# Kernel optimization log

Measured on AMD Instinct MI355X. Metric: run time of the kernel, lower is better.

Reference implementation:

```python
import jax, jax.numpy as jnp
import numpy as np

B, S, D, H, NS = 4, 4096, 1024, 16, 128
DA, DF = 512, 4096
DK, DV = DA // H, D // H  # 32, 64
TEMP = 1.0
EPS = 1e-6


def setup_inputs() -> dict:
    key = jax.random.key(0)
    ks = jax.random.split(key, 8)
    r = lambda k, shp: jax.random.normal(k, shp, jnp.float32) * 0.02
    return dict(
        x=jax.random.normal(ks[0], (B, S, D), jnp.float32),
        mask=jnp.ones((B, S), jnp.float32),
        residual_scale=jnp.ones((1,), jnp.float32),
        w_q=r(ks[1], (D, DA)), b_q=jnp.zeros((DA,), jnp.float32),
        w_kv=r(ks[2], (D, DA + D)), b_kv=jnp.zeros((DA + D,), jnp.float32),
        w_s=r(ks[3], (D, H * NS)), b_s=jnp.zeros((H * NS,), jnp.float32),
        w_cat=r(ks[4], (D, D)), b_cat=jnp.zeros((D,), jnp.float32),
        norm1_w=jnp.ones((D,), jnp.float32), norm2_w=jnp.ones((D,), jnp.float32),
        w1=r(ks[5], (D, DF)), b1=jnp.zeros((DF,), jnp.float32),
        w2=r(ks[6], (DF, D)), b2=jnp.zeros((D,), jnp.float32),
    )


def _rms(x, w):
    return x * jax.lax.rsqrt(jnp.mean(x * x, axis=-1, keepdims=True) + EPS) * w


def _forward(x, mask, residual_scale, w_q, b_q, w_kv, b_kv, w_s, b_s,
             w_cat, b_cat, norm1_w, norm2_w, w1, b1, w2, b2):
    neg = jnp.finfo(jnp.float32).min
    xn = _rms(x, norm1_w)
    q = (xn @ w_q + b_q).reshape(B, S, H, DK).transpose(0, 2, 1, 3)        # [B,H,S,DK]
    kv = (xn @ w_kv + b_kv).reshape(B, S, H, DK + DV).transpose(0, 2, 1, 3)  # [B,H,S,DK+DV]
    k_raw, v_raw = kv[..., :DK], kv[..., DK:]

    # DSZRC sampler: per-head soft routing of S tokens -> NS sampled KV rows
    logits = (x @ w_s + b_s).reshape(B, S, H, NS).transpose(0, 2, 3, 1)    # [B,H,NS,S]
    logits = jnp.where(mask[:, None, None, :] > 0, logits, neg)
    probs = jax.nn.softmax(logits / TEMP, axis=-1)
    kv_s = jnp.einsum('bhms,bhsd->bhmd', probs, kv)                        # [B,H,NS,DK+DV]
    k_s, v_s = kv_s[..., :DK], kv_s[..., DK:]

    # branch 1: dense SDPA over sampled KV
    scale = 1.0 / np.sqrt(DK).astype(np.float32)
    att = jax.nn.softmax(jnp.einsum('bhqd,bhkd->bhqk', q, k_s) * scale, axis=-1)
    out1 = jnp.einsum('bhqk,bhkd->bhqd', att, v_s)                         # [B,H,S,DV]

    # branch 2: fp16 sliding-window flash attn, left window = NS (keys i-NS..i)
    f16 = lambda t: t.astype(jnp.float16).astype(jnp.float32)
    qh, kh, vh = f16(q), f16(k_raw), f16(v_raw)
    bs = NS
    nb = S // bs
    qb = qh.reshape(B, H, nb, bs, DK)
    kb = kh.reshape(B, H, nb, bs, DK)
    vb = vh.reshape(B, H, nb, bs, DV)
    shift = lambda t: jnp.concatenate([jnp.zeros_like(t[:, :, :1]), t[:, :, :-1]], axis=2)
    kctx = jnp.concatenate([shift(kb), kb], axis=3)                        # [B,H,nb,2bs,DK]
    vctx = jnp.concatenate([shift(vb), vb], axis=3)
    sc = jnp.einsum('bhnad,bhnkd->bhnak', qb, kctx) * scale                # [B,H,nb,bs,2bs]
    a = jnp.arange(bs)[:, None]
    bcol = jnp.arange(2 * bs)[None, :]
    band = (bcol >= a) & (bcol <= a + NS)                                  # 0 <= q-k <= NS
    tpos = jnp.arange(nb)[:, None, None]
    valid = band[None] & ((tpos > 0) | (bcol >= bs)[None])                 # no keys before pos 0
    p = jax.nn.softmax(jnp.where(valid[None, None], sc, neg), axis=-1)
    out2 = f16(jnp.einsum('bhnak,bhnkd->bhnad', p, vctx)).reshape(B, H, S, DV)

    x_att = (out1 + out2).transpose(0, 2, 1, 3).reshape(B, S, D)
    x = x + (x_att @ w_cat + b_cat) * residual_scale
    h = _rms(x, norm2_w)
    x = x + (jax.nn.gelu(h @ w1 + b1, approximate=False) @ w2 + b2) * residual_scale
    return x


def reference(x, mask, residual_scale, w_q, b_q, w_kv, b_kv, w_s, b_s,
              w_cat, b_cat, norm1_w, norm2_w, w1, b1, w2, b2):
    return _forward(x, mask, residual_scale, w_q, b_q, w_kv, b_kv, w_s, b_s,
                    w_cat, b_cat, norm1_w, norm2_w, w1, b1, w2, b2)
```

## Files before the change

kernel.cpp:

```cpp
#include <hip/hip_runtime.h>
#include <cstdint>
#include <cmath>

#define DEV __device__ __forceinline__

using f16 = _Float16;
typedef f16  f16x4 __attribute__((ext_vector_type(4)));
typedef f16  f16x8 __attribute__((ext_vector_type(8)));
typedef float f32x4 __attribute__((ext_vector_type(4)));

constexpr int Bq = 4, Sq = 4096, Hq = 16;
constexpr int Tq = Bq * Sq;

DEV void gload_lds16(const void* g, void* l) {
  __builtin_amdgcn_global_load_lds(
      (const __attribute__((address_space(1))) void*)g,
      (__attribute__((address_space(3))) void*)l, 16, 0, 0);
}

DEV void stage_swz(const char* gbase, long gstride, char* lds, int nbytes,
                   int rowlog, int swzmask) {
  int tid = threadIdx.x;
  for (int b0 = 0; b0 < nbytes; b0 += 4096) {
    int P = b0 + tid * 16;
    int L = P ^ (((P >> rowlog) & swzmask) << 4);
    long row  = L >> rowlog;
    int  colb = L & ((1 << rowlog) - 1);
    gload_lds16(gbase + row * gstride + colb, lds + b0 + (tid & ~63) * 16);
  }
}

DEV void stage_swz512(const char* gbase, long gstride, char* lds, int nbytes,
                      int rowlog, int swzmask) {
  int tid = threadIdx.x;
  for (int b0 = 0; b0 < nbytes; b0 += 8192) {
    int P = b0 + tid * 16;
    int L = P ^ (((P >> rowlog) & swzmask) << 4);
    long row  = L >> rowlog;
    int  colb = L & ((1 << rowlog) - 1);
    gload_lds16(gbase + row * gstride + colb, lds + b0 + (tid & ~63) * 16);
  }
}

DEV float wave16_max(float v) {
#pragma unroll
  for (int d = 1; d < 16; d <<= 1) v = fmaxf(v, __shfl_xor(v, d, 64));
  return v;
}
DEV float wave16_sum(float v) {
#pragma unroll
  for (int d = 1; d < 16; d <<= 1) v += __shfl_xor(v, d, 64);
  return v;
}

__global__ __launch_bounds__(256) void wcast_k(const float* __restrict__ W,
                                               f16* __restrict__ Wt, int K, int N) {
  int n0 = blockIdx.x * 32, k0 = blockIdx.y * 32;
  __shared__ float tile[32][33];
  int tid = threadIdx.x, r = tid >> 5, c = tid & 31;
#pragma unroll
  for (int i = 0; i < 4; ++i)
    tile[r + i * 8][c] = W[(size_t)(k0 + r + i * 8) * N + n0 + c];
  __syncthreads();
#pragma unroll
  for (int i = 0; i < 4; ++i) {
    int rr = r + i * 8;
    Wt[(size_t)(n0 + rr) * K + k0 + c] = (f16)tile[c][rr];
  }
}

__global__ void bias_concat_k(const float* __restrict__ bq, const float* __restrict__ bkv,
                              float* __restrict__ out) {
  int i = blockIdx.x * 256 + threadIdx.x;
  out[i] = (i < 512) ? bq[i] : bkv[i - 512];
}

__global__ __launch_bounds__(256) void rmsnorm_k(const float* __restrict__ x,
                                                 const float* __restrict__ w,
                                                 f16* __restrict__ xn) {
  int row = blockIdx.x, tid = threadIdx.x;
  float4 v = ((const float4*)(x + (size_t)row * 1024))[tid];
  float ss = v.x * v.x + v.y * v.y + v.z * v.z + v.w * v.w;
#pragma unroll
  for (int d = 1; d < 64; d <<= 1) ss += __shfl_xor(ss, d, 64);
  __shared__ float red[4];
  if ((tid & 63) == 0) red[tid >> 6] = ss;
  __syncthreads();
  float tot = red[0] + red[1] + red[2] + red[3];
  float r = rsqrtf(tot * (1.0f / 1024.0f) + 1e-6f);
  float4 wv = ((const float4*)w)[tid];
  f16x4 o;
  o[0] = (f16)(v.x * r * wv.x); o[1] = (f16)(v.y * r * wv.y);
  o[2] = (f16)(v.z * r * wv.z); o[3] = (f16)(v.w * r * wv.w);
  *(f16x4*)(xn + (size_t)row * 1024 + tid * 4) = o;
}

template <int MODE>
__global__ __launch_bounds__(256) void gemm_k(const f16* __restrict__ A, const f16* __restrict__ Bt,
                                              const float* __restrict__ bias,
                                              float* __restrict__ outF,
                                              const float* __restrict__ resid,
                                              const float* __restrict__ rsp,
                                              int M, int N, int K, int lda, int ldb) {
  __shared__ alignas(16) char smA[2][16384];
  __shared__ alignas(16) char smB[2][16384];
  int nwgx = gridDim.x, nbc = gridDim.y;
  int bidl = blockIdx.y * nwgx + blockIdx.x;
  int cpx = (nwgx * nbc) >> 3;
  int xcd = bidl & 7, pos = bidl >> 3;
  int rpm = cpx / nbc;
  int nbi = pos / rpm, mbi = pos % rpm;
  int mb = xcd * rpm + mbi;
  long n0 = (long)nbi * 128;
  int tid = threadIdx.x, lane = tid & 63, wv = tid >> 6, wr = wv >> 1, wc = wv & 1;
  long m0 = (long)mb * 128;
  f32x4 acc[4][4] = {};
  const char* Ab = (MODE == 7) ? nullptr : (const char*)(A + m0 * lda);
  const char* Bb = (const char*)(Bt + n0 * ldb);

  auto stageAB = [&](int buf, int k0) {
    stage_swz(Bb + (long)k0 * 2, (long)ldb * 2, smB[buf], 16384, 7, 7);
    if (MODE == 7) {
      const char* Ab7 = (const char*)(A + (((m0 >> 12) * 16 + (k0 >> 6)) * 4096 + (m0 & 4095)) * 64);
      stage_swz(Ab7, 128, smA[buf], 16384, 7, 7);
    } else {
      stage_swz(Ab + (long)k0 * 2, (long)lda * 2, smA[buf], 16384, 7, 7);
    }
  };

  stageAB(0, 0);
  __syncthreads();
  int cur = 0;
  for (int k0 = 0; k0 < K; k0 += 64) {
    if (k0 + 64 < K) stageAB(cur ^ 1, k0 + 64);
#pragma unroll
    for (int kk = 0; kk < 2; ++kk) {
      int kbyte = kk * 64 + (lane >> 4) * 16;
      f16x8 aF[4], bF[4];
#pragma unroll
      for (int m = 0; m < 4; ++m) {
        int L = (wr * 64 + m * 16 + (lane & 15)) * 128 + kbyte;
        aF[m] = *(const f16x8*)(smA[cur] + (L ^ (((L >> 7) & 7) << 4)));
      }
#pragma unroll
      for (int n = 0; n < 4; ++n) {
        int L = (wc * 64 + n * 16 + (lane & 15)) * 128 + kbyte;
        bF[n] = *(const f16x8*)(smB[cur] + (L ^ (((L >> 7) & 7) << 4)));
      }
#pragma unroll
      for (int m = 0; m < 4; ++m)
#pragma unroll
        for (int n = 0; n < 4; ++n)
          acc[m][n] = __builtin_amdgcn_mfma_f32_16x16x32_f16(aF[m], bF[n], acc[m][n], 0, 0, 0);
    }
    __syncthreads();
    cur ^= 1;
  }
  float rsv = rsp[0];
#pragma unroll
  for (int m = 0; m < 4; ++m)
#pragma unroll
    for (int n = 0; n < 4; ++n) {
      long gn = n0 + wc * 64 + n * 16 + (lane & 15);
      float bv = bias[gn];
      long rbase = m0 + wr * 64 + m * 16 + (lane >> 4) * 4;
#pragma unroll
      for (int i = 0; i < 4; ++i) {
        long gm = rbase + i;
        float v = acc[m][n][i] + bv;
        long idx = gm * N + gn;
        outF[idx] = resid[idx] + v * rsv;
      }
    }
}

template <int MODE>
__global__ __launch_bounds__(512) void gemm256_k(const f16* __restrict__ A, const f16* __restrict__ Bt,
                                                 const float* __restrict__ bias,
                                                 f16* __restrict__ o1, f16* __restrict__ o2,
                                                 f16* __restrict__ o3,
                                                 const float* __restrict__ resid,
                                                 int M, int N, int K, int lda, int ldb, int pp) {
  __shared__ alignas(16) char smA[2][32768];
  __shared__ alignas(16) char smB[2][32768];
  int nwgx = gridDim.x, nbc = gridDim.y;
  int bidl = blockIdx.y * nwgx + blockIdx.x;
  int cpx = (nwgx * nbc) >> 3;
  int xcd = bidl & 7, pos = bidl >> 3;
  int rpm = cpx / nbc;
  int nbi = pos / rpm, mbi = pos % rpm;
  int mb = xcd * rpm + mbi;
  long n0 = (long)nbi * 256;
  int tid = threadIdx.x, lane = tid & 63, wv = tid >> 6;
  int wr = wv >> 2, wc = wv & 3;
  long m0;
  long t0 = 0;
  int bq = 0;
  if (MODE == 5) {
    bq = mb >> 3; int sb = mb & 7;
    m0 = (long)sb * 256;
    t0 = (long)bq * 4096 + (long)pp * 2048 + m0;
  } else {
    m0 = (long)mb * 256;
  }
  f32x4 acc[8][4] = {};
  const char* Ab = (MODE == 5) ? nullptr : (const char*)(A + m0 * lda);
  const char* Bb = (const char*)(Bt + n0 * ldb);

  auto stageAB = [&](int buf, int k0) {
    stage_swz512(Bb + (long)k0 * 2, (long)ldb * 2, smB[buf], 32768, 7, 7);
    if (MODE == 5) {
      int P = tid * 16;
#pragma unroll
      for (int b0 = 0; b0 < 32768; b0 += 8192) {
        int PP = b0 + P;
        int L = PP ^ (((PP >> 7) & 7) << 4);
        int row = L >> 7, colf = (L & 127) >> 1;
        const float* src = resid + (size_t)(t0 + row) * 1024 + k0 + colf;
        float4 u0 = *(const float4*)src;
        float4 u1 = *(const float4*)(src + 4);
        f16x8 o;
        o[0] = (f16)u0.x; o[1] = (f16)u0.y; o[2] = (f16)u0.z; o[3] = (f16)u0.w;
        o[4] = (f16)u1.x; o[5] = (f16)u1.y; o[6] = (f16)u1.z; o[7] = (f16)u1.w;
        *(f16x8*)(smA[buf] + PP) = o;
      }
    } else {
      stage_swz512(Ab + (long)k0 * 2, (long)lda * 2, smA[buf], 32768, 7, 7);
    }
  };

  stageAB(0, 0);
  __syncthreads();
  int cur = 0;
  for (int k0 = 0; k0 < K; k0 += 64) {
    if (k0 + 64 < K) stageAB(cur ^ 1, k0 + 64);
#pragma unroll
    for (int kk = 0; kk < 2; ++kk) {
      int kbyte = kk * 64 + (lane >> 4) * 16;
      f16x8 aF[8], bF[4];
#pragma unroll
      for (int m = 0; m < 8; ++m) {
        int L = (wr * 128 + m * 16 + (lane & 15)) * 128 + kbyte;
        aF[m] = *(const f16x8*)(smA[cur] + (L ^ (((L >> 7) & 7) << 4)));
      }
#pragma unroll
      for (int n = 0; n < 4; ++n) {
        int L = (wc * 64 + n * 16 + (lane & 15)) * 128 + kbyte;
        bF[n] = *(const f16x8*)(smB[cur] + (L ^ (((L >> 7) & 7) << 4)));
      }
#pragma unroll
      for (int m = 0; m < 8; ++m)
#pragma unroll
        for (int n = 0; n < 4; ++n)
          acc[m][n] = __builtin_amdgcn_mfma_f32_16x16x32_f16(aF[m], bF[n], acc[m][n], 0, 0, 0);
    }
    __syncthreads();
    cur ^= 1;
  }
#pragma unroll
  for (int m = 0; m < 8; ++m)
#pragma unroll
    for (int n = 0; n < 4; ++n) {
      long gn = n0 + wc * 64 + n * 16 + (lane & 15);
      float bv = bias[gn];
      long rbase = m0 + wr * 128 + m * 16 + (lane >> 4) * 4;
      if (MODE == 4) {
        long b = rbase >> 12, s = rbase & 4095;
        if (gn < 512) {
          long h = gn >> 5, dk = gn & 31;
#pragma unroll
          for (int i = 0; i < 4; ++i)
            o1[(((size_t)b * 16 + h) * 4096 + s + i) * 32 + dk] = (f16)(acc[m][n][i] + bv);
        } else {
          long c2 = gn - 512, h = c2 / 96, j = c2 % 96;
          if (j < 32) {
#pragma unroll
            for (int i = 0; i < 4; ++i)
              o2[(((size_t)b * 16 + h) * 4096 + s + i) * 32 + j] = (f16)(acc[m][n][i] + bv);
          } else {
            f16x4 pk;
#pragma unroll
            for (int i = 0; i < 4; ++i) pk[i] = (f16)(acc[m][n][i] + bv);
            *(f16x4*)(o3 + (((size_t)b * 16 + h) * 64 + (j - 32)) * 4096 + s) = pk;
          }
        }
      } else {
#pragma unroll
        for (int i = 0; i < 4; ++i) {
          long gm = rbase + i;
          float v = acc[m][n][i] + bv;
          if (MODE == 3) {
            float u = v * 0.7978845608028654f * (1.f + 0.044715f * v * v);
            float e = __expf(fminf(2.f * u, 80.f));
            o1[gm * N + gn] = (f16)(v * (e / (e + 1.f)));
          } else {
            o1[((size_t)bq * 2048 + gn) * 2048 + gm] = (f16)v;
          }
        }
      }
    }
}

__global__ __launch_bounds__(256) void kvs_k(const f16* __restrict__ lt,
                                             const f16* __restrict__ kh,
                                             const f16* __restrict__ vT,
                                             const float* __restrict__ mask,
                                             float* __restrict__ pacc, int pass) {
  int gx = blockIdx.x, nsb = gx & 3, sc = gx >> 2;
  int h = blockIdx.y, b = blockIdx.z;
  int bh = b * 16 + h;
  __shared__ alignas(16) char smA[4096];
  __shared__ alignas(16) f16 smB[112][88];
  int tid = threadIdx.x, lane = tid & 63, w = tid >> 6;
  int mf = w >> 1, nb0 = (w & 1) * 4, nfr = (w & 1) ? 3 : 4;
  for (int idx = tid; idx < 16 * 64; idx += 256) {
    int r = 96 + (idx >> 6), c2 = idx & 63;
    smB[r][c2] = (r == 96) ? (f16)1.0f : (f16)0.0f;
  }
  f32x4 acc[4] = {};
  const f16* ltb = lt + ((size_t)bh * 128 + nsb * 32) * 2048;
  for (int it = 0; it < 4; ++it) {
    int sl0 = sc * 256 + it * 64;
    int s0g = pass * 2048 + sl0;
    __syncthreads();
    {
      int P = tid * 16;
      int L = P ^ (((P >> 7) & 7) << 4);
      int row = L >> 7, colf = (L & 127) >> 1;
      f16x8 lv = *(const f16x8*)(ltb + (size_t)row * 2048 + sl0 + colf);
      const float* mrow = mask + (size_t)b * 4096 + s0g + colf;
      float4 m0v = *(const float4*)mrow, m1v = *(const float4*)(mrow + 4);
      float mm[8] = {m0v.x, m0v.y, m0v.z, m0v.w, m1v.x, m1v.y, m1v.z, m1v.w};
      f16x8 o;
#pragma unroll
      for (int j = 0; j < 8; ++j)
        o[j] = (f16)((mm[j] > 0.f) ? expf((float)lv[j] - 8.0f) : 0.0f);
      *(f16x8*)(smA + P) = o;
    }
    {
      int sl = tid >> 2, jg = (tid & 3) * 8;
      f16x8 u = *(const f16x8*)(kh + ((size_t)bh * 4096 + s0g + sl) * 32 + jg);
#pragma unroll
      for (int j = 0; j < 8; ++j) smB[jg + j][sl] = u[j];
    }
#pragma unroll
    for (int half = 0; half < 2; ++half) {
      int task = tid + half * 256;
      int dv = task >> 3, sl0v = (task & 7) * 8;
      f16x8 u = *(const f16x8*)(vT + ((size_t)bh * 64 + dv) * 4096 + s0g + sl0v);
      *(f16x8*)(&smB[32 + dv][sl0v]) = u;
    }
    __syncthreads();
#pragma unroll
    for (int kk = 0; kk < 2; ++kk) {
      int kbyte = kk * 64 + (lane >> 4) * 16;
      int L = (mf * 16 + (lane & 15)) * 128 + kbyte;
      f16x8 aF = *(const f16x8*)(smA + (L ^ (((L >> 7) & 7) << 4)));
#pragma unroll
      for (int n = 0; n < 4; ++n)
        if (n < nfr) {
          f16x8 bF = *(const f16x8*)((const char*)smB + ((nb0 + n) * 16 + (lane & 15)) * 176 + kbyte);
          acc[n] = __builtin_amdgcn_mfma_f32_16x16x32_f16(aF, bF, acc[n], 0, 0, 0);
        }
    }
  }
  int slot = pass * 8 + sc;
  float* pb = pacc + (((size_t)bh * 4 + nsb) * 16 + slot) * 3584;
#pragma unroll
  for (int n = 0; n < 4; ++n)
    if (n < nfr) {
      int col = (nb0 + n) * 16 + (lane & 15);
#pragma unroll
      for (int i = 0; i < 4; ++i) {
        int nsrow = mf * 16 + (lane >> 4) * 4 + i;
        pb[(size_t)nsrow * 112 + col] = acc[n][i];
      }
    }
}

__global__ __launch_bounds__(256) void kvs_fin_k(const float* __restrict__ pacc,
                                                 f16* __restrict__ ks, f16* __restrict__ vst) {
  int bh = blockIdx.x, tid = threadIdx.x;
  __shared__ float den[128];
  const float* base = pacc + (size_t)bh * 4 * 16 * 3584;
  if (tid < 128) {
    int nsb = tid >> 5, nsl = tid & 31;
    float d = 0.f;
#pragma unroll
    for (int slot = 0; slot < 16; ++slot)
      d += base[((size_t)nsb * 16 + slot) * 3584 + (size_t)nsl * 112 + 96];
    den[tid] = d;
  }
  __syncthreads();
  for (int e = tid; e < 12288; e += 256) {
    int ns = e / 96, j = e % 96;
    int nsb = ns >> 5, nsl = ns & 31;
    float sv = 0.f;
#pragma unroll
    for (int slot = 0; slot < 16; ++slot)
      sv += base[((size_t)nsb * 16 + slot) * 3584 + (size_t)nsl * 112 + j];
    float v = sv / den[ns];
    if (j < 32) ks[((size_t)bh * 128 + ns) * 32 + j] = (f16)v;
    else        vst[((size_t)bh * 64 + (j - 32)) * 128 + ns] = (f16)v;
  }
}

__global__ __launch_bounds__(256) void att_k(const f16* __restrict__ qh,
                                             const f16* __restrict__ kh,
                                             const f16* __restrict__ vTh,
                                             const f16* __restrict__ ksb,
                                             const f16* __restrict__ vstb,
                                             f16* __restrict__ xatt) {
  int ntj = blockIdx.x, h = blockIdx.y, b = blockIdx.z;
  int nt = ((ntj & 7) << 3) | (ntj >> 3);
  int bh = b * 16 + h, s0 = nt * 64;
  __shared__ alignas(16) char smQ[4096];
  __shared__ alignas(16) char smK[4096];
  __shared__ alignas(16) char smV[8192];
  __shared__ alignas(16) f16 smP[4][16][72];
  int tid = threadIdx.x, lane = tid & 63, w = tid >> 6;
  const float scale = 0.17677669529663687f;
  stage_swz((const char*)(qh + ((size_t)bh * 4096 + s0) * 32), 64, smQ, 4096, 6, 3);

  float mrun[4], lrun[4], m1[4], l1[4];
#pragma unroll
  for (int i = 0; i < 4; ++i) { mrun[i] = -1e30f; lrun[i] = 0.f; m1[i] = -1e30f; l1[i] = 0.f; }
  f32x4 o2[4] = {}, o1[4] = {};

  for (int c = 0; c < 5; ++c) {
    bool win = (c < 3);
    long kb = (long)s0 + (c - 2) * 64;
    if (win && kb < 0) continue;
    __syncthreads();
    if (win) {
      stage_swz((const char*)(kh + ((size_t)bh * 4096 + kb) * 32), 64, smK, 4096, 6, 3);
      stage_swz((const char*)(vTh + (size_t)bh * 64 * 4096 + kb), 8192, smV, 8192, 7, 7);
    } else {
      int sc = c - 3;
      stage_swz((const char*)(ksb + ((size_t)bh * 128 + sc * 64) * 32), 64, smK, 4096, 6, 3);
      stage_swz((const char*)(vstb + (size_t)bh * 64 * 128 + sc * 64), 256, smV, 8192, 7, 7);
    }
    __syncthreads();
    f32x4 s[4] = {};
    {
      int kbyte = (lane >> 4) * 16;
      int Lq = (w * 16 + (lane & 15)) * 64 + kbyte;
      f16x8 aF = *(const f16x8*)(smQ + (Lq ^ (((Lq >> 6) & 3) << 4)));
#pragma unroll
      for (int n = 0; n < 4; ++n) {
        int Lk = (n * 16 + (lane & 15)) * 64 + kbyte;
        f16x8 bF = *(const f16x8*)(smK + (Lk ^ (((Lk >> 6) & 3) << 4)));
        s[n] = __builtin_amdgcn_mfma_f32_16x16x32_f16(aF, bF, s[n], 0, 0, 0);
      }
    }
    float* mr = win ? mrun : m1;
    float* lr = win ? lrun : l1;
    f32x4* oo = win ? o2 : o1;
#pragma unroll
    for (int i = 0; i < 4; ++i) {
      int a2 = w * 16 + (lane >> 4) * 4 + i;
      float nm = mr[i];
#pragma unroll
      for (int n = 0; n < 4; ++n) {
        int kl = n * 16 + (lane & 15);
        bool valid = !win || (c == 1) || (c == 0 ? (kl >= a2) : (kl <= a2));
        float v = valid ? s[n][i] * scale : -1e30f;
        s[n][i] = v; nm = fmaxf(nm, v);
      }
      nm = wave16_max(nm);
      float alpha = expf(mr[i] - nm);
      float sum = 0.f;
#pragma unroll
      for (int n = 0; n < 4; ++n) { float p = expf(s[n][i] - nm); s[n][i] = p; sum += p; }
      sum = wave16_sum(sum);
      lr[i] = lr[i] * alpha + sum;
      mr[i] = nm;
#pragma unroll
      for (int n = 0; n < 4; ++n) oo[n][i] *= alpha;
    }
#pragma unroll
    for (int n = 0; n < 4; ++n)
#pragma unroll
      for (int i = 0; i < 4; ++i)
        smP[w][(lane >> 4) * 4 + i][n * 16 + (lane & 15)] = (f16)s[n][i];
#pragma unroll
    for (int kk = 0; kk < 2; ++kk) {
      int kb2 = kk * 64 + (lane >> 4) * 16;
      f16x8 aP = *(const f16x8*)((const char*)smP[w] + (lane & 15) * 144 + kb2);
#pragma unroll
      for (int n = 0; n < 4; ++n) {
        int dv = n * 16 + (lane & 15);
        int Lv = dv * 128 + kb2;
        f16x8 bV = *(const f16x8*)(smV + (Lv ^ (((Lv >> 7) & 7) << 4)));
        oo[n] = __builtin_amdgcn_mfma_f32_16x16x32_f16(aP, bV, oo[n], 0, 0, 0);
      }
    }
  }
  f16* xb = xatt + ((size_t)bh * 4096 + s0) * 64;
#pragma unroll
  for (int n = 0; n < 4; ++n)
#pragma unroll
    for (int i = 0; i < 4; ++i) {
      int row = w * 16 + (lane >> 4) * 4 + i, dv = n * 16 + (lane & 15);
      xb[(size_t)row * 64 + dv] = (f16)(o2[n][i] / lrun[i] + o1[n][i] / l1[i]);
    }
}

__global__ void sentinel_k(float* out, size_t n, float val) {
  size_t i = (size_t)blockIdx.x * 256 + threadIdx.x;
  size_t stride = (size_t)gridDim.x * 256;
  for (; i < n; i += stride) out[i] = val;
}

constexpr size_t OFF_WQKV = 0;
constexpr size_t OFF_WSC  = OFF_WQKV + 2048ull * 1024 * 2;
constexpr size_t OFF_WCAT = OFF_WSC  + 2048ull * 1024 * 2;
constexpr size_t OFF_W1   = OFF_WCAT + 1024ull * 1024 * 2;
constexpr size_t OFF_W2   = OFF_W1   + 4096ull * 1024 * 2;
constexpr size_t OFF_BQKV = OFF_W2   + 1024ull * 4096 * 2;
constexpr size_t OFF_ZB   = OFF_BQKV + 8192;
constexpr size_t OFF_Q    = OFF_ZB   + 4096;
constexpr size_t OFF_K    = OFF_Q    + (size_t)Tq * 512 * 2;
constexpr size_t OFF_P1   = OFF_K    + (size_t)Tq * 512 * 2;
constexpr size_t OFF_VT   = OFF_P1   + (size_t)Tq * 1024 * 2;
constexpr size_t OFF_KVA  = OFF_VT   + (size_t)Tq * 1024 * 2;
constexpr size_t OFF_KS   = OFF_KVA  + 64ull * 128 * 112 * 4;
constexpr size_t OFF_VST  = OFF_KS   + 64ull * 128 * 32 * 2;
constexpr size_t WS_NEED  = OFF_VST  + 64ull * 64 * 128 * 2;

extern "C" void kernel_launch(void* const* d_in, const int* in_sizes, int n_in,
                              void* d_out, int out_size, void* d_ws, size_t ws_size,
                              hipStream_t stream) {
  float* xo = (float*)d_out;
  if (ws_size < WS_NEED) {
    float val = -(1000.0f + (float)(ws_size / 1000000ull));
    sentinel_k<<<2048, 256, 0, stream>>>(xo, (size_t)out_size, val);
    return;
  }
  const float* x     = (const float*)d_in[0];
  const float* mask  = (const float*)d_in[1];
  const float* rsp   = (const float*)d_in[2];
  const float* w_q   = (const float*)d_in[3];
  const float* b_q   = (const float*)d_in[4];
  const float* w_kv  = (const float*)d_in[5];
  const float* b_kv  = (const float*)d_in[6];
  const float* w_s   = (const float*)d_in[7];
  const float* b_s   = (const float*)d_in[8];
  const float* w_cat = (const float*)d_in[9];
  const float* b_cat = (const float*)d_in[10];
  const float* n1w   = (const float*)d_in[11];
  const float* n2w   = (const float*)d_in[12];
  const float* w1    = (const float*)d_in[13];
  const float* b1    = (const float*)d_in[14];
  const float* w2    = (const float*)d_in[15];
  const float* b2    = (const float*)d_in[16];
  char* ws = (char*)d_ws;

  f16*   wqkv_t = (f16*)(ws + OFF_WQKV);
  f16*   ws_t   = (f16*)(ws + OFF_WSC);
  f16*   wcat_t = (f16*)(ws + OFF_WCAT);
  f16*   w1_t   = (f16*)(ws + OFF_W1);
  f16*   w2_t   = (f16*)(ws + OFF_W2);
  float* bqkv   = (float*)(ws + OFF_BQKV);
  f16*   q_h    = (f16*)(ws + OFF_Q);
  f16*   k_h    = (f16*)(ws + OFF_K);
  f16*   h_h    = (f16*)(ws + OFF_Q);
  f16*   xn_h   = (f16*)(ws + OFF_P1);
  f16*   lt16   = (f16*)(ws + OFF_P1);
  f16*   xatt_h = (f16*)(ws + OFF_P1);
  f16*   g_h    = (f16*)(ws + OFF_P1);
  f16*   vT_h   = (f16*)(ws + OFF_VT);
  f16*   ks_h   = (f16*)(ws + OFF_KS);
  f16*   vst_h  = (f16*)(ws + OFF_VST);

  wcast_k<<<dim3(16, 32),  256, 0, stream>>>(w_q,   wqkv_t,              1024, 512);
  wcast_k<<<dim3(48, 32),  256, 0, stream>>>(w_kv,  wqkv_t + 512 * 1024, 1024, 1536);
  wcast_k<<<dim3(64, 32),  256, 0, stream>>>(w_s,   ws_t,                1024, 2048);
  wcast_k<<<dim3(32, 32),  256, 0, stream>>>(w_cat, wcat_t,              1024, 1024);
  wcast_k<<<dim3(128, 32), 256, 0, stream>>>(w1,    w1_t,                1024, 4096);
  wcast_k<<<dim3(32, 128), 256, 0, stream>>>(w2,    w2_t,                4096, 1024);
  bias_concat_k<<<8, 256, 0, stream>>>(b_q, b_kv, bqkv);

  rmsnorm_k<<<Tq, 256, 0, stream>>>(x, n1w, xn_h);
  gemm256_k<4><<<dim3(64, 8), 512, 0, stream>>>(xn_h, wqkv_t, bqkv, q_h, k_h, vT_h,
                                                nullptr, Tq, 2048, 1024, 1024, 1024, 0);
  for (int p = 0; p < 2; ++p) {
    gemm256_k<5><<<dim3(32, 8), 512, 0, stream>>>(nullptr, ws_t, b_s, lt16, nullptr, nullptr,
                                                  x, 8192, 2048, 1024, 0, 1024, p);
    kvs_k<<<dim3(32, 16, 4), 256, 0, stream>>>(lt16, k_h, vT_h, mask, xo, p);
  }
  kvs_fin_k<<<64, 256, 0, stream>>>(xo, ks_h, vst_h);
  att_k<<<dim3(64, 16, 4), 256, 0, stream>>>(q_h, k_h, vT_h, ks_h, vst_h, xatt_h);
  gemm_k<7><<<dim3(128, 8), 256, 0, stream>>>(xatt_h, wcat_t, b_cat, xo,
                                              x, rsp, Tq, 1024, 1024, 0, 1024);
  rmsnorm_k<<<Tq, 256, 0, stream>>>(xo, n2w, h_h);
  for (int mc = 0; mc < 2; ++mc) {
    const f16* hA = h_h + (size_t)mc * 8192 * 1024;
    float* xoc = xo + (size_t)mc * 8192 * 1024;
    gemm256_k<3><<<dim3(32, 16), 512, 0, stream>>>(hA, w1_t, b1, g_h, nullptr, nullptr,
                                                   nullptr, 8192, 4096, 1024, 1024, 1024, 0);
    gemm_k<2><<<dim3(64, 8), 256, 0, stream>>>(g_h, w2_t, b2, xoc,
                                               xoc, rsp, 8192, 1024, 4096, 4096, 4096);
  }
}
```

Baseline: 924.4 us.

## Restructure GEMM mainloops to keep two async LDS stages in flight

Replaces the simple double-buffer loop (stage next, compute, __syncthreads) in two GEMM kernels with a schedule that issues two tile loads up front and waits with explicit vmcnt counts. Each buffer is refilled two steps ahead, and sched_barrier-wrapped s_barrier calls replace __syncthreads. The goal is to hide global-to-LDS load latency behind MFMA work by keeping a full stage of loads outstanding. MODE 5, which stages A with register float-to-half conversion, keeps the old loop. The vmcnt(8) constant must match the exact number of loads each stage issues, which is fragile.

```diff
diff --git a/kernel.cpp b/kernel.cpp
--- a/kernel.cpp
+++ b/kernel.cpp
@@ -40,6 +40,13 @@
     int  colb = L & ((1 << rowlog) - 1);
     gload_lds16(gbase + row * gstride + colb, lds + b0 + (tid & ~63) * 16);
   }
+}
+
+DEV void pipe_barrier() {
+  __builtin_amdgcn_sched_barrier(0);
+  __builtin_amdgcn_s_barrier();
+  asm volatile("" ::: "memory");
+  __builtin_amdgcn_sched_barrier(0);
 }
 
 DEV float wave16_max(float v) {
@@ -127,12 +134,7 @@
       stage_swz(Ab + (long)k0 * 2, (long)lda * 2, smA[buf], 16384, 7, 7);
     }
   };
-
-  stageAB(0, 0);
-  __syncthreads();
-  int cur = 0;
-  for (int k0 = 0; k0 < K; k0 += 64) {
-    if (k0 + 64 < K) stageAB(cur ^ 1, k0 + 64);
+  auto doCompute = [&](const char* cA, const char* cB) {
 #pragma unroll
     for (int kk = 0; kk < 2; ++kk) {
       int kbyte = kk * 64 + (lane >> 4) * 16;
@@ -140,12 +142,12 @@
 #pragma unroll
       for (int m = 0; m < 4; ++m) {
         int L = (wr * 64 + m * 16 + (lane & 15)) * 128 + kbyte;
-        aF[m] = *(const f16x8*)(smA[cur] + (L ^ (((L >> 7) & 7) << 4)));
+        aF[m] = *(const f16x8*)(cA + (L ^ (((L >> 7) & 7) << 4)));
       }
 #pragma unroll
       for (int n = 0; n < 4; ++n) {
         int L = (wc * 64 + n * 16 + (lane & 15)) * 128 + kbyte;
-        bF[n] = *(const f16x8*)(smB[cur] + (L ^ (((L >> 7) & 7) << 4)));
+        bF[n] = *(const f16x8*)(cB + (L ^ (((L >> 7) & 7) << 4)));
       }
 #pragma unroll
       for (int m = 0; m < 4; ++m)
@@ -153,8 +155,23 @@
         for (int n = 0; n < 4; ++n)
           acc[m][n] = __builtin_amdgcn_mfma_f32_16x16x32_f16(aF[m], bF[n], acc[m][n], 0, 0, 0);
     }
-    __syncthreads();
-    cur ^= 1;
+  };
+
+  int T = K >> 6;
+  stageAB(0, 0);
+  stageAB(1, 64);
+  asm volatile("s_waitcnt vmcnt(8)" ::: "memory");
+  pipe_barrier();
+  for (int t = 0; t < T; ++t) {
+    doCompute(smA[t & 1], smB[t & 1]);
+    pipe_barrier();
+    if (t + 2 < T) {
+      stageAB(t & 1, (t + 2) << 6);
+      asm volatile("s_waitcnt vmcnt(8)" ::: "memory");
+    } else {
+      asm volatile("s_waitcnt vmcnt(0)" ::: "memory");
+    }
+    if (t + 1 < T) pipe_barrier();
   }
   float rsv = rsp[0];
 #pragma unroll
@@ -228,12 +245,7 @@
       stage_swz512(Ab + (long)k0 * 2, (long)lda * 2, smA[buf], 32768, 7, 7);
     }
   };
-
-  stageAB(0, 0);
-  __syncthreads();
-  int cur = 0;
-  for (int k0 = 0; k0 < K; k0 += 64) {
-    if (k0 + 64 < K) stageAB(cur ^ 1, k0 + 64);
+  auto doCompute = [&](const char* cA, const char* cB) {
 #pragma unroll
     for (int kk = 0; kk < 2; ++kk) {
       int kbyte = kk * 64 + (lane >> 4) * 16;
@@ -241,12 +253,12 @@
 #pragma unroll
       for (int m = 0; m < 8; ++m) {
         int L = (wr * 128 + m * 16 + (lane & 15)) * 128 + kbyte;
-        aF[m] = *(const f16x8*)(smA[cur] + (L ^ (((L >> 7) & 7) << 4)));
+        aF[m] = *(const f16x8*)(cA + (L ^ (((L >> 7) & 7) << 4)));
       }
 #pragma unroll
       for (int n = 0; n < 4; ++n) {
         int L = (wc * 64 + n * 16 + (lane & 15)) * 128 + kbyte;
-        bF[n] = *(const f16x8*)(smB[cur] + (L ^ (((L >> 7) & 7) << 4)));
+        bF[n] = *(const f16x8*)(cB + (L ^ (((L >> 7) & 7) << 4)));
       }
 #pragma unroll
       for (int m = 0; m < 8; ++m)
@@ -254,8 +266,35 @@
         for (int n = 0; n < 4; ++n)
           acc[m][n] = __builtin_amdgcn_mfma_f32_16x16x32_f16(aF[m], bF[n], acc[m][n], 0, 0, 0);
     }
+  };
+
+  if constexpr (MODE == 5) {
+    stageAB(0, 0);
     __syncthreads();
-    cur ^= 1;
+    int cur = 0;
+    for (int k0 = 0; k0 < K; k0 += 64) {
+      if (k0 + 64 < K) stageAB(cur ^ 1, k0 + 64);
+      doCompute(smA[cur], smB[cur]);
+      __syncthreads();
+      cur ^= 1;
+    }
+  } else {
+    int T = K >> 6;
+    stageAB(0, 0);
+    stageAB(1, 64);
+    asm volatile("s_waitcnt vmcnt(8)" ::: "memory");
+    pipe_barrier();
+    for (int t = 0; t < T; ++t) {
+      doCompute(smA[t & 1], smB[t & 1]);
+      pipe_barrier();
+      if (t + 2 < T) {
+        stageAB(t & 1, (t + 2) << 6);
+        asm volatile("s_waitcnt vmcnt(8)" ::: "memory");
+      } else {
+        asm volatile("s_waitcnt vmcnt(0)" ::: "memory");
+      }
+      if (t + 1 < T) pipe_barrier();
+    }
   }
 #pragma unroll
   for (int m = 0; m < 8; ++m)
```

Result: slower. 949.8 us (+2.8%).
